# Optimization experiments

Hardware: AMD Instinct MI355X
Metric: run time of the kernel (lower is better)

## Reference

```python
import jax, jax.numpy as jnp
import numpy as np

N_NODES = 50000
N_EDGES = 300000
N_REL = 8
D = 256
N_LAYERS = 3


def setup_inputs() -> dict:
    key = jax.random.key(0)
    k1, k2, k3, k4, k5 = jax.random.split(key, 5)
    x = jax.random.normal(k1, (N_NODES, D), dtype=jnp.float32)
    # Glorot-ish scaling to keep activations sane through relu/sigmoid
    scale = 1.0 / np.sqrt(D)
    weights = jax.random.normal(k2, (N_LAYERS, N_REL, D, D), dtype=jnp.float32) * scale
    roots = jax.random.normal(k3, (N_LAYERS, D, D), dtype=jnp.float32) * scale
    biases = jnp.zeros((N_LAYERS, D), dtype=jnp.float32)
    edge_index = jax.random.randint(k4, (2, N_EDGES), 0, N_NODES, dtype=jnp.int64)
    edge_type = jax.random.randint(k5, (N_EDGES,), 0, N_REL, dtype=jnp.int64)
    return {"x": x, "weights": weights, "roots": roots, "biases": biases,
            "edge_index": edge_index, "edge_type": edge_type}


def _rgcn_layer(x, W, root, bias, src, dst, seg):
    # PyG RGCNConv (aggr='add'): per relation, sum neighbor features into dst,
    # then apply that relation's weight. Vectorized: segment key = rel*N + dst.
    agg = jax.ops.segment_sum(x[src], seg, num_segments=N_REL * N_NODES)  # [R*N, d]
    agg = agg.reshape(N_REL, N_NODES, -1)                                  # [R, N, d]
    return jnp.einsum('rnd,rde->ne', agg, W) + x @ root + bias


def reference(x, weights, roots, biases, edge_index, edge_type):
    src, dst = edge_index[0], edge_index[1]
    seg = edge_type * N_NODES + dst  # combined (relation, dst) segment id
    h = x
    for l in range(N_LAYERS - 1):
        h = jax.nn.relu(_rgcn_layer(h, weights[l], roots[l], biases[l], src, dst, seg))
    h = jax.nn.sigmoid(_rgcn_layer(h, weights[-1], roots[-1], biases[-1], src, dst, seg))
    return h
```

## Files before the change

kernel.cpp:

```cpp
#include <hip/hip_runtime.h>
#include <hip/hip_bf16.h>
#include <cstdint>
#include <cstddef>

#define D 256
#define RNUM 8
#define LAYERS 3
#define SEGS 9
#define KSTEPS 8
#define BM 64
#define NWAVE 8
#define AST 264
#define SMASK 0x03FFFFFF

typedef _Float16 f16x8 __attribute__((ext_vector_type(8)));
typedef float f32x4  __attribute__((ext_vector_type(4)));

__device__ __forceinline__ unsigned short f2h(float f) {
    union { _Float16 h; unsigned short u; } x;
    x.h = (_Float16)f;
    return x.u;
}
__device__ __forceinline__ float h2f(unsigned short u) {
    union { _Float16 h; unsigned short u; } x;
    x.u = u;
    return (float)x.h;
}

__device__ __forceinline__ void wave_barrier() {
    asm volatile("s_waitcnt lgkmcnt(0)" ::: "memory");
    __builtin_amdgcn_s_barrier();
    asm volatile("" ::: "memory");
    __builtin_amdgcn_sched_barrier(0);
}


__global__ void zero_kernel(int* __restrict__ p, int n) {
    int i = blockIdx.x * blockDim.x + threadIdx.x;
    if (i < n) p[i] = 0;
}

__global__ void detect_kernel(const int* __restrict__ ei32, int* __restrict__ flag) {
    __shared__ int allzero;
    if (threadIdx.x == 0) allzero = 1;
    __syncthreads();
    if (ei32[2 * threadIdx.x + 1] != 0) allzero = 0;
    __syncthreads();
    if (threadIdx.x == 0) flag[0] = allzero;
}

__device__ __forceinline__ void load_edge(const void* ei, const void* et, int flg,
                                          int e, int E, int N,
                                          int& s, int& d, int& r) {
    if (flg) {
        const long long* a = (const long long*)ei;
        const long long* b = (const long long*)et;
        s = (int)a[e]; d = (int)a[E + e]; r = (int)b[e];
    } else {
        const int* a = (const int*)ei;
        const int* b = (const int*)et;
        s = a[e]; d = a[E + e]; r = b[e];
    }
    if ((unsigned)s >= (unsigned)N) s = 0;
    if ((unsigned)d >= (unsigned)N) d = 0;
    if ((unsigned)r >= (unsigned)RNUM) r = 0;
}

__global__ void count_kernel(const void* __restrict__ ei, const void* __restrict__ et,
                             const int* __restrict__ flag, int* __restrict__ pp,
                             int E, int N) {
    int e = blockIdx.x * blockDim.x + threadIdx.x;
    if (e >= E) return;
    int s, d, r;
    load_edge(ei, et, flag[0], e, E, N, s, d, r);
    atomicAdd(&pp[r * N + d], 1);
}

__global__ void scan_blocks_kernel(int* __restrict__ pp, int* __restrict__ bsum, int n) {
    __shared__ int sb[1024];
    const int t = threadIdx.x;
    const int i = blockIdx.x * 1024 + t;
    const int v = (i < n) ? pp[i] : 0;
    sb[t] = v;
    __syncthreads();
    for (int off = 1; off < 1024; off <<= 1) {
        int x = 0;
        if (t >= off) x = sb[t - off];
        __syncthreads();
        if (t >= off) sb[t] += x;
        __syncthreads();
    }
    if (i < n) pp[i] = sb[t] - v;
    if (t == 1023) bsum[blockIdx.x] = sb[t];
}

__global__ void scan_sums_kernel(int* __restrict__ bsum, int nb) {
    __shared__ int sb[512];
    const int t = threadIdx.x;
    const int v = (t < nb) ? bsum[t] : 0;
    sb[t] = v;
    __syncthreads();
    for (int off = 1; off < 512; off <<= 1) {
        int x = 0;
        if (t >= off) x = sb[t - off];
        __syncthreads();
        if (t >= off) sb[t] += x;
        __syncthreads();
    }
    if (t < nb) bsum[t] = sb[t] - v;
}

__global__ void scan_add_kernel(int* __restrict__ pp, const int* __restrict__ bsum,
                                int n, int E) {
    const int i = blockIdx.x * 1024 + threadIdx.x;
    if (i < n) pp[i] += bsum[blockIdx.x];
    if (i == 0) pp[n] = E;
}

__global__ void fill_kernel(const void* __restrict__ ei, const void* __restrict__ et,
                            const int* __restrict__ flag, const int* __restrict__ pp,
                            int* __restrict__ cur, int* __restrict__ epk,
                            int E, int N) {
    int e = blockIdx.x * blockDim.x + threadIdx.x;
    if (e >= E) return;
    int s, d, r;
    load_edge(ei, et, flag[0], e, E, N, s, d, r);
    const int key = r * N + d;
    const int pos = atomicAdd(&cur[key], 1);
    const int slot = pp[key] + pos;
    if ((unsigned)slot < (unsigned)E)
        epk[slot] = ((d & (BM - 1)) << 26) | (s & SMASK);
}

__global__ void wconvert_kernel(const float* __restrict__ weights,
                                const float* __restrict__ roots,
                                unsigned short* __restrict__ wblk) {
    const int total = LAYERS * SEGS * KSTEPS * 256 * 32;
    int idx = blockIdx.x * blockDim.x + threadIdx.x;
    if (idx >= total) return;
    const int kk  = idx & 31;
    const int col = (idx >> 5) & 255;
    const int ks  = (idx >> 13) & 7;
    const int sl  = idx >> 16;
    const int seg = sl % SEGS, l = sl / SEGS;
    const int krow = ks * 32 + kk;
    float v;
    if (seg == 0)
        v = roots[((size_t)l * 256 + krow) * 256 + col];
    else
        v = weights[(((size_t)l * RNUM + (seg - 1)) * 256 + krow) * 256 + col];
    const unsigned short hi = f2h(v);
    const unsigned short lo = f2h(v - h2f(hi));
    const size_t base = ((size_t)sl * KSTEPS + ks) * 16384;
    wblk[base + (size_t)col * 32 + kk] = hi;
    wblk[base + 8192 + (size_t)col * 32 + kk] = lo;
}

template <int ACT>
__global__ __launch_bounds__(512, 4)
void layer_kernel(const float* __restrict__ hin,
                  const unsigned short* __restrict__ wl,
                  const float* __restrict__ bias,
                  const int* __restrict__ pp,
                  const int* __restrict__ epk,
                  float* __restrict__ hout,
                  int N) {
    __shared__ unsigned short Ahi[BM * AST];

    const int tid = threadIdx.x;
    const int wv = tid >> 6;
    const int lane = tid & 63;
    const int lm = lane & 15;
    const int lq = lane >> 4;
    const int rb = blockIdx.x * BM;
    const int cbase = wv * 32 + lm;

    f32x4 acc[4][2];
#pragma unroll
    for (int i = 0; i < 4; ++i)
#pragma unroll
        for (int j = 0; j < 2; ++j) acc[i][j] = (f32x4)0.f;

    int bnd = 0;
    if (lane < 16) {
        const int r = lane >> 1;
        int row = rb + wv * 8 + ((lane & 1) << 3);
        if (row > N) row = N;
        bnd = pp[r * N + row];
    }

    auto flushrow = [&](int row, const float4& s) {
        ushort4 h4;
        h4.x = f2h(s.x); h4.y = f2h(s.y);
        h4.z = f2h(s.z); h4.w = f2h(s.w);
        *reinterpret_cast<ushort4*>(&Ahi[row * AST + lane * 4]) = h4;
    };

    for (int m = wv; m < BM; m += NWAVE) {
        int r = rb + m;
        if (r >= N) r = N - 1;
        const float4 v = *reinterpret_cast<const float4*>(hin + (size_t)r * D + lane * 4);
        ushort4 h4;
        h4.x = f2h(v.x); h4.y = f2h(v.y);
        h4.z = f2h(v.z); h4.w = f2h(v.w);
        *reinterpret_cast<ushort4*>(&Ahi[m * AST + lane * 4]) = h4;
    }

    int nbeg = __builtin_amdgcn_readlane(bnd, 0);
    int ncnt = __builtin_amdgcn_readlane(bnd, 1) - nbeg;
    int ep = 0;
    { const int c = ncnt < 64 ? ncnt : 64; if (lane < c) ep = epk[nbeg + lane]; }

    wave_barrier();

    for (int seg = 0; seg < SEGS; ++seg) {
        const unsigned short* wseg = wl + (size_t)seg * KSTEPS * 16384;
        for (int ks = 0; ks < KSTEPS; ++ks) {
            const unsigned short* wks = wseg + (size_t)ks * 16384;
            f16x8 bh[2], bl[2];
#pragma unroll
            for (int ct = 0; ct < 2; ++ct) {
                const int c = cbase + ct * 16;
                bh[ct] = *reinterpret_cast<const f16x8*>(wks + (size_t)c * 32 + lq * 8);
                bl[ct] = *reinterpret_cast<const f16x8*>(wks + 8192 + (size_t)c * 32 + lq * 8);
            }
            f16x8 ah[4];
#pragma unroll
            for (int rt = 0; rt < 4; ++rt) {
                const int off = (rt * 16 + lm) * AST + ks * 32 + lq * 8;
                ah[rt] = *reinterpret_cast<const f16x8*>(&Ahi[off]);
            }
#pragma unroll
            for (int rt = 0; rt < 4; ++rt)
#pragma unroll
                for (int ct = 0; ct < 2; ++ct) {
                    acc[rt][ct] = __builtin_amdgcn_mfma_f32_16x16x32_f16(
                        ah[rt], bl[ct], acc[rt][ct], 0, 0, 0);
                    acc[rt][ct] = __builtin_amdgcn_mfma_f32_16x16x32_f16(
                        ah[rt], bh[ct], acc[rt][ct], 0, 0, 0);
                }
        }

        if (seg + 1 < SEGS) {
            wave_barrier();

#pragma unroll
            for (int m = 0; m < 8; ++m) {
                const int row = wv * 8 + m;
                *reinterpret_cast<ushort4*>(&Ahi[row * AST + lane * 4]) =
                    make_ushort4(0, 0, 0, 0);
            }

            {
                const int beg = nbeg, cnt = ncnt;
                int e0 = ep;
                int cur = -1;
                float4 sum = make_float4(0.f, 0.f, 0.f, 0.f);
                int processed = 0;
                while (processed < cnt) {
                    int avail = cnt - processed;
                    if (avail > 64) avail = 64;
                    int inner = 0;
                    while (inner < avail) {
                        const int take = (avail - inner) < 8 ? (avail - inner) : 8;
                        int pk[8]; float4 u[8];
#pragma unroll
                        for (int i = 0; i < 8; ++i) {
                            if (i < take) {
                                pk[i] = __builtin_amdgcn_readlane(e0, inner + i);
                                const int s = pk[i] & SMASK;
                                u[i] = *reinterpret_cast<const float4*>(
                                    hin + (size_t)s * D + lane * 4);
                            }
                        }
#pragma unroll
                        for (int i = 0; i < 8; ++i) {
                            if (i < take) {
                                const int lr = (int)(((unsigned)pk[i]) >> 26);
                                if (lr != cur) {
                                    if (cur >= 0) flushrow(cur, sum);
                                    sum = make_float4(0.f, 0.f, 0.f, 0.f);
                                    cur = lr;
                                }
                                sum.x += u[i].x; sum.y += u[i].y;
                                sum.z += u[i].z; sum.w += u[i].w;
                            }
                        }
                        inner += take;
                    }
                    processed += avail;
                    if (processed < cnt) {
                        int c = cnt - processed; if (c > 64) c = 64;
                        e0 = 0;
                        if (lane < c) e0 = epk[beg + processed + lane];
                    }
                }
                if (cur >= 0) flushrow(cur, sum);
            }

            if (seg + 2 < SEGS) {
                nbeg = __builtin_amdgcn_readlane(bnd, (seg + 1) * 2);
                ncnt = __builtin_amdgcn_readlane(bnd, (seg + 1) * 2 + 1) - nbeg;
                ep = 0;
                const int c = ncnt < 64 ? ncnt : 64;
                if (lane < c) ep = epk[nbeg + lane];
            }

            wave_barrier();
        }
    }

#pragma unroll
    for (int ct = 0; ct < 2; ++ct) {
        const int col = wv * 32 + ct * 16 + lm;
        const float bb = bias[col];
#pragma unroll
        for (int rt = 0; rt < 4; ++rt) {
#pragma unroll
            for (int i = 0; i < 4; ++i) {
                const int row = rb + rt * 16 + lq * 4 + i;
                if (row < N) {
                    float z = acc[rt][ct][i] + bb;
                    z = (ACT == 0) ? fmaxf(z, 0.f) : 1.f / (1.f + __expf(-z));
                    hout[(size_t)row * D + col] = z;
                }
            }
        }
    }
}

extern "C" void kernel_launch(void* const* d_in, const int* in_sizes, int n_in,
                              void* d_out, int out_size, void* d_ws, size_t ws_size,
                              hipStream_t stream) {
    const float* x       = (const float*)d_in[0];
    const float* weights = (const float*)d_in[1];
    const float* roots   = (const float*)d_in[2];
    const float* biases  = (const float*)d_in[3];
    const void*  ei      = d_in[4];
    const void*  et      = d_in[5];

    const int N = in_sizes[0] / D;
    const int E = in_sizes[4] / 2;
    const int NP = N * RNUM;

    char* ws = (char*)d_ws;
    int* flag = (int*)ws;
    int* pp   = (int*)(ws + 256);
    int* cur  = pp + (NP + 1);
    int* bsum = cur + NP;
    int* epk  = bsum + 512;
    size_t hoff = (256 + (size_t)(NP + 1 + NP + 512 + E) * 4 + 255) & ~(size_t)255;
    float* h1 = (float*)(ws + hoff);
    unsigned short* wblk = (unsigned short*)(ws + hoff + (size_t)N * D * sizeof(float));

    const int wtotal = LAYERS * SEGS * KSTEPS * 256 * 32;
    wconvert_kernel<<<(wtotal + 255) / 256, 256, 0, stream>>>(weights, roots, wblk);

    detect_kernel<<<1, 256, 0, stream>>>((const int*)ei, flag);
    const int zn = 2 * NP + 513;
    zero_kernel<<<(zn + 255) / 256, 256, 0, stream>>>(pp, zn);
    const int eb = (E + 255) / 256;
    count_kernel<<<eb, 256, 0, stream>>>(ei, et, flag, pp, E, N);
    const int nb = (NP + 1023) / 1024;
    scan_blocks_kernel<<<nb, 1024, 0, stream>>>(pp, bsum, NP);
    scan_sums_kernel<<<1, 512, 0, stream>>>(bsum, nb);
    scan_add_kernel<<<nb, 1024, 0, stream>>>(pp, bsum, NP, E);
    fill_kernel<<<eb, 256, 0, stream>>>(ei, et, flag, pp, cur, epk, E, N);

    const int tiles = (N + BM - 1) / BM;
    const size_t wlayer = (size_t)SEGS * KSTEPS * 16384;
    const float* hin = x;
    for (int l = 0; l < LAYERS; ++l) {
        float* hout = (l == 1) ? h1 : (float*)d_out;
        const unsigned short* wlp = wblk + (size_t)l * wlayer;
        const float* bl = biases + (size_t)l * D;
        if (l == LAYERS - 1)
            layer_kernel<1><<<tiles, 512, 0, stream>>>(hin, wlp, bl, pp, epk, hout, N);
        else
            layer_kernel<0><<<tiles, 512, 0, stream>>>(hin, wlp, bl, pp, epk, hout, N);
        hin = hout;
    }
}
```

Measured before the change: 732.1 us.

## Prefetch first gathered neighbor rows and next edge chunk before MFMA loop

Before each segment's MFMA loop, the kernel now issues global loads for the first up-to-8 neighbor rows of the next segment's gather, and also the next segment's edge-packet indices. A sched_barrier keeps these loads ahead of the matrix work, so their latency overlaps with compute instead of stalling the gather phase. The cost is extra live vector registers (8 float4 plus indices) held across the MFMA loop, which may lower occupancy or cause spills.

```diff
diff --git a/kernel.cpp b/kernel.cpp
--- a/kernel.cpp
+++ b/kernel.cpp
@@ -214,6 +214,28 @@
     wave_barrier();
 
     for (int seg = 0; seg < SEGS; ++seg) {
+        float4 u[8];
+        int upto = 0;
+        if (seg + 1 < SEGS) {
+            upto = ncnt < 8 ? ncnt : 8;
+#pragma unroll
+            for (int i = 0; i < 8; ++i) {
+                if (i < upto) {
+                    const int s = __builtin_amdgcn_readlane(ep, i) & SMASK;
+                    u[i] = *reinterpret_cast<const float4*>(
+                        hin + (size_t)s * D + lane * 4);
+                }
+            }
+        }
+        int nbeg2 = 0, ncnt2 = 0, ep2 = 0;
+        if (seg + 2 < SEGS) {
+            nbeg2 = __builtin_amdgcn_readlane(bnd, (seg + 1) * 2);
+            ncnt2 = __builtin_amdgcn_readlane(bnd, (seg + 1) * 2 + 1) - nbeg2;
+            const int c = ncnt2 < 64 ? ncnt2 : 64;
+            if (lane < c) ep2 = epk[nbeg2 + lane];
+        }
+        __builtin_amdgcn_sched_barrier(0);
+
         const unsigned short* wseg = wl + (size_t)seg * KSTEPS * 16384;
         for (int ks = 0; ks < KSTEPS; ++ks) {
             const unsigned short* wks = wseg + (size_t)ks * 16384;
@@ -253,23 +275,38 @@
 
             {
                 const int beg = nbeg, cnt = ncnt;
-                int e0 = ep;
                 int cur = -1;
                 float4 sum = make_float4(0.f, 0.f, 0.f, 0.f);
+#pragma unroll
+                for (int i = 0; i < 8; ++i) {
+                    if (i < upto) {
+                        const int pkv = __builtin_amdgcn_readlane(ep, i);
+                        const int lr = (int)(((unsigned)pkv) >> 26);
+                        if (lr != cur) {
+                            if (cur >= 0) flushrow(cur, sum);
+                            sum = make_float4(0.f, 0.f, 0.f, 0.f);
+                            cur = lr;
+                        }
+                        sum.x += u[i].x; sum.y += u[i].y;
+                        sum.z += u[i].z; sum.w += u[i].w;
+                    }
+                }
+                int e0 = ep;
                 int processed = 0;
+                int innerStart = upto;
                 while (processed < cnt) {
                     int avail = cnt - processed;
                     if (avail > 64) avail = 64;
-                    int inner = 0;
+                    int inner = innerStart;
                     while (inner < avail) {
                         const int take = (avail - inner) < 8 ? (avail - inner) : 8;
-                        int pk[8]; float4 u[8];
+                        int pk[8]; float4 w[8];
 #pragma unroll
                         for (int i = 0; i < 8; ++i) {
                             if (i < take) {
                                 pk[i] = __builtin_amdgcn_readlane(e0, inner + i);
                                 const int s = pk[i] & SMASK;
-                                u[i] = *reinterpret_cast<const float4*>(
+                                w[i] = *reinterpret_cast<const float4*>(
                                     hin + (size_t)s * D + lane * 4);
                             }
                         }
@@ -282,13 +319,14 @@
                                     sum = make_float4(0.f, 0.f, 0.f, 0.f);
                                     cur = lr;
                                 }
-                                sum.x += u[i].x; sum.y += u[i].y;
-                                sum.z += u[i].z; sum.w += u[i].w;
+                                sum.x += w[i].x; sum.y += w[i].y;
+                                sum.z += w[i].z; sum.w += w[i].w;
                             }
                         }
                         inner += take;
                     }
                     processed += avail;
+                    innerStart = 0;
                     if (processed < cnt) {
                         int c = cnt - processed; if (c > 64) c = 64;
                         e0 = 0;
@@ -298,13 +336,7 @@
                 if (cur >= 0) flushrow(cur, sum);
             }
 
-            if (seg + 2 < SEGS) {
-                nbeg = __builtin_amdgcn_readlane(bnd, (seg + 1) * 2);
-                ncnt = __builtin_amdgcn_readlane(bnd, (seg + 1) * 2 + 1) - nbeg;
-                ep = 0;
-                const int c = ncnt < 64 ? ncnt : 64;
-                if (lane < c) ep = epk[nbeg + lane];
-            }
+            nbeg = nbeg2; ncnt = ncnt2; ep = ep2;
 
             wave_barrier();
         }
```

Measured after the change: 968.1 us. +32.2%, slower.
